# Kernel optimization log

Hardware: AMD Instinct MI355X
Metric: run time of the kernel (lower is better)

## Reference

```python
import jax, jax.numpy as jnp
import numpy as np

B, S, C, OUT = 8, 2048, 1024, 1024

def setup_inputs() -> dict:
    key = jax.random.key(0)
    ks = jax.random.split(key, 10)
    s = C ** -0.5
    return {
        "input": jax.random.normal(ks[0], (B, S, C), jnp.float32),
        "memory": jax.random.normal(ks[1], (B, S, C), jnp.float32),
        "Wq": jax.random.normal(ks[2], (C, C), jnp.float32) * s,
        "bq": jnp.zeros((C,), jnp.float32),
        "Wk": jax.random.normal(ks[3], (C, C), jnp.float32) * s,
        "bk": jnp.zeros((C,), jnp.float32),
        "Wv": jax.random.normal(ks[4], (C, C), jnp.float32) * s,
        "bv": jnp.zeros((C,), jnp.float32),
        "Wo": jax.random.normal(ks[5], (OUT, C), jnp.float32) * s,
        "bo": jnp.zeros((OUT,), jnp.float32),
    }

def reference(input, memory, Wq, bq, Wk, bk, Wv, bv, Wo, bo):
    depth_scale = input.shape[2] ** -0.5
    q = (input @ Wq.T + bq) * depth_scale          # [B, Sq, C]
    k = memory @ Wk.T + bk                          # [B, Sk, C]
    v = memory @ Wv.T + bv                          # [B, Sk, C]
    logit = jnp.einsum('bqc,bkc->bqk', q, k)        # [B, Sq, Sk]
    attn = jax.nn.softmax(logit, axis=-1)
    sel = jnp.einsum('bqk,bkc->bqc', attn, v)       # [B, Sq, C]
    return sel @ Wo.T + bo                          # [B, Sq, OUT]
```

## Files before the change

### kernel.cpp

```cpp
#include <hip/hip_runtime.h>
#include <hip/hip_bf16.h>


typedef __attribute__((ext_vector_type(8))) short short8;
typedef __attribute__((ext_vector_type(4))) float f32x4;

static __device__ __forceinline__ unsigned short f2bf(float f) {
  union { float f; unsigned u; } x; x.f = f;
  unsigned r = x.u + 0x7FFFu + ((x.u >> 16) & 1u);
  return (unsigned short)(r >> 16);
}

static __device__ __forceinline__ void g2l16(const void* g, void* l) {
  __builtin_amdgcn_global_load_lds(
      (const __attribute__((address_space(1))) void*)g,
      (__attribute__((address_space(3))) void*)l, 16, 0, 0);
}

__global__ __launch_bounds__(256) void cvt_kernel(const float* __restrict__ in,
                                                  unsigned short* __restrict__ out,
                                                  long long n4) {
  long long i = (long long)blockIdx.x * 256 + threadIdx.x;
  const long long stride = (long long)gridDim.x * 256;
  for (; i < n4; i += stride) {
    float4 v = ((const float4*)in)[i];
    ushort4 o;
    o.x = f2bf(v.x); o.y = f2bf(v.y); o.z = f2bf(v.z); o.w = f2bf(v.w);
    ((ushort4*)out)[i] = o;
  }
}

#define EPI_BF16 0
#define EPI_BF16_TRANS 1
#define EPI_EXP 2
#define EPI_PV 3
#define EPI_F32 4

template <int BM, int BN, int WM, int WN, int EPI, bool HAS_BIAS>
__global__ __launch_bounds__(512, 2) void gemm_kernel(
    const unsigned short* __restrict__ A, const unsigned short* __restrict__ B,
    const float* __restrict__ bias, void* __restrict__ Dv,
    int K, int lda, int ldb, int ldd,
    long long sA, long long sB, long long sD, float scale) {
  constexpr int MF = BM / (WM * 16);
  constexpr int NF = BN / (WN * 16);
  constexpr int LA = BM / 128;
  constexpr int LB = BN / 128;
  constexpr int LT = LA + LB;

  int lin = blockIdx.x + gridDim.x * (blockIdx.y + gridDim.y * blockIdx.z);
  const int nwg = gridDim.x * gridDim.y * gridDim.z;
  lin = (lin & 7) * (nwg >> 3) + (lin >> 3);
  const int bx = lin % gridDim.x;
  int rem0 = lin / gridDim.x;
  const int by = rem0 % gridDim.y;
  const int bz = rem0 / gridDim.y;

  const int bm = bx * BM;
  const int bn = by * BN;
  const int tid = threadIdx.x;
  const int lane = tid & 63;
  const int wid = tid >> 6;
  const int wr = (wid / WN) * (BM / WM);
  const int wc = (wid % WN) * (BN / WN);
  const int fr = lane & 15;
  const int hi = lane >> 4;

  __shared__ __align__(16) unsigned short As[4][BM * 32];
  __shared__ __align__(16) unsigned short Bs[4][BN * 32];

  f32x4 acc[MF][NF];
#pragma unroll
  for (int m = 0; m < MF; ++m)
#pragma unroll
    for (int n = 0; n < NF; ++n) acc[m][n] = (f32x4){0.f, 0.f, 0.f, 0.f};

  f32x4 asum[MF];
  short8 ones;
#pragma unroll
  for (int m = 0; m < MF; ++m) asum[m] = (f32x4){0.f, 0.f, 0.f, 0.f};
#pragma unroll
  for (int j = 0; j < 8; ++j) ones[j] = (short)0x3F80;

  const unsigned short* Abase = A + (long long)bz * sA;
  const unsigned short* Bbase = B + (long long)bz * sB;

  auto stage = [&](int tt) {
    const int buf = tt & 3;
#pragma unroll
    for (int i = 0; i < LA; ++i) {
      const int slot = i * 512 + tid;
      const int row = slot >> 2;
      const int gs = (slot & 3) ^ ((row >> 1) & 3);
      g2l16(Abase + (long long)(bm + row) * lda + tt * 32 + gs * 8,
            &As[buf][slot * 8]);
    }
#pragma unroll
    for (int i = 0; i < LB; ++i) {
      const int slot = i * 512 + tid;
      const int row = slot >> 2;
      const int gs = (slot & 3) ^ ((row >> 1) & 3);
      g2l16(Bbase + (long long)(bn + row) * ldb + tt * 32 + gs * 8,
            &Bs[buf][slot * 8]);
    }
  };

  const int NT = K >> 5;

  stage(0); stage(1); stage(2);

  const int glx = (fr >> 1) & 3;

  for (int t = 0; t < NT; ++t) {
    const int ahead = NT - 1 - t;
    if (ahead >= 2) {
      if (LT == 4) asm volatile("s_waitcnt vmcnt(8)" ::: "memory");
      else         asm volatile("s_waitcnt vmcnt(6)" ::: "memory");
    } else if (ahead == 1) {
      if (LT == 4) asm volatile("s_waitcnt vmcnt(4)" ::: "memory");
      else         asm volatile("s_waitcnt vmcnt(3)" ::: "memory");
    } else {
      asm volatile("s_waitcnt vmcnt(0)" ::: "memory");
    }
    __builtin_amdgcn_s_barrier();
    __builtin_amdgcn_sched_barrier(0);

    if (t + 3 < NT) stage(t + 3);

    const int buf = t & 3;
    short8 af[MF], bf[NF];
#pragma unroll
    for (int m = 0; m < MF; ++m) {
      const int row = wr + m * 16 + fr;
      af[m] = *(const short8*)&As[buf][row * 32 + ((hi ^ glx) << 3)];
    }
#pragma unroll
    for (int n = 0; n < NF; ++n) {
      const int row = wc + n * 16 + fr;
      bf[n] = *(const short8*)&Bs[buf][row * 32 + ((hi ^ glx) << 3)];
    }
#pragma unroll
    for (int m = 0; m < MF; ++m)
#pragma unroll
      for (int n = 0; n < NF; ++n)
        acc[m][n] = __builtin_amdgcn_mfma_f32_16x16x32_bf16(af[m], bf[n],
                                                            acc[m][n], 0, 0, 0);
    if (EPI == EPI_PV) {
#pragma unroll
      for (int m = 0; m < MF; ++m)
        asum[m] = __builtin_amdgcn_mfma_f32_16x16x32_bf16(af[m], ones,
                                                          asum[m], 0, 0, 0);
    }
    __builtin_amdgcn_sched_barrier(0);
    __builtin_amdgcn_s_barrier();
  }

  const int cr = hi * 4;
  const int cc = fr;
#pragma unroll
  for (int m = 0; m < MF; ++m) {
    const int row0 = bm + wr + m * 16 + cr;
#pragma unroll
    for (int n = 0; n < NF; ++n) {
      const int col = bn + wc + n * 16 + cc;
      const float bv = HAS_BIAS ? bias[col] : 0.f;
      if (EPI == EPI_F32) {
        float* D = (float*)Dv + (long long)bz * sD;
#pragma unroll
        for (int j = 0; j < 4; ++j)
          D[(long long)(row0 + j) * ldd + col] = acc[m][n][j] + bv;
      } else if (EPI == EPI_BF16) {
        unsigned short* D = (unsigned short*)Dv + (long long)bz * sD;
#pragma unroll
        for (int j = 0; j < 4; ++j)
          D[(long long)(row0 + j) * ldd + col] = f2bf((acc[m][n][j] + bv) * scale);
      } else if (EPI == EPI_BF16_TRANS) {
        unsigned short* D = (unsigned short*)Dv + (long long)bz * sD;
        ushort4 pk;
        pk.x = f2bf((acc[m][n][0] + bv) * scale);
        pk.y = f2bf((acc[m][n][1] + bv) * scale);
        pk.z = f2bf((acc[m][n][2] + bv) * scale);
        pk.w = f2bf((acc[m][n][3] + bv) * scale);
        *(ushort4*)&D[(long long)col * ldd + row0] = pk;
      } else if (EPI == EPI_EXP) {
        unsigned short* D = (unsigned short*)Dv + (long long)bz * sD;
#pragma unroll
        for (int j = 0; j < 4; ++j)
          D[(long long)(row0 + j) * ldd + col] = f2bf(__expf(acc[m][n][j]));
      } else {
        unsigned short* D = (unsigned short*)Dv + (long long)bz * sD;
#pragma unroll
        for (int j = 0; j < 4; ++j) {
          const float li = 1.f / asum[m][j];
          D[(long long)(row0 + j) * ldd + col] = f2bf(acc[m][n][j] * li);
        }
      }
    }
  }
}

extern "C" void kernel_launch(void* const* d_in, const int* in_sizes, int n_in,
                              void* d_out, int out_size, void* d_ws, size_t ws_size,
                              hipStream_t stream) {
  (void)in_sizes; (void)n_in; (void)out_size;
  const float* input  = (const float*)d_in[0];
  const float* memory = (const float*)d_in[1];
  const float* Wq = (const float*)d_in[2];
  const float* bq = (const float*)d_in[3];
  const float* Wk = (const float*)d_in[4];
  const float* bk = (const float*)d_in[5];
  const float* Wv = (const float*)d_in[6];
  const float* bv = (const float*)d_in[7];
  const float* Wo = (const float*)d_in[8];
  const float* bo = (const float*)d_in[9];
  float* out = (float*)d_out;

  const int S = 2048, C = 1024;
  const int CB = 4;
  const long long BS = 16384;
  const long long N_IN = BS * C;
  const long long N_W  = (long long)C * C;

  char* p = (char*)d_ws;
  auto alloc = [&](size_t bytes) {
    char* r = p;
    p += (bytes + 255) & ~(size_t)255;
    return r;
  };
  unsigned short* wqb  = (unsigned short*)alloc(N_W * 2);
  unsigned short* wkb  = (unsigned short*)alloc(N_W * 2);
  unsigned short* wvb  = (unsigned short*)alloc(N_W * 2);
  unsigned short* wob  = (unsigned short*)alloc(N_W * 2);
  unsigned short* Qb   = (unsigned short*)alloc(N_IN * 2);
  unsigned short* Kb   = (unsigned short*)alloc(N_IN * 2);
  unsigned short* Xb   = (unsigned short*)alloc(N_IN * 2);
  if ((size_t)(p - (char*)d_ws) > ws_size) return;

  unsigned short* Vt  = (unsigned short*)d_out;
  unsigned short* inb = (unsigned short*)d_out + N_IN;
  unsigned short* memb = Xb;
  unsigned short* Pt   = Xb;

  cvt_kernel<<<1024, 256, 0, stream>>>(Wq, wqb, N_W / 4);
  cvt_kernel<<<1024, 256, 0, stream>>>(Wk, wkb, N_W / 4);
  cvt_kernel<<<1024, 256, 0, stream>>>(Wv, wvb, N_W / 4);
  cvt_kernel<<<1024, 256, 0, stream>>>(Wo, wob, N_W / 4);
  cvt_kernel<<<2048, 256, 0, stream>>>(memory, memb, N_IN / 4);
  cvt_kernel<<<2048, 256, 0, stream>>>(input,  inb,  N_IN / 4);

  const float depth_scale = 0.03125f;

  gemm_kernel<256, 256, 2, 4, EPI_BF16, true><<<dim3(64, 4, 1), 512, 0, stream>>>(
      memb, wkb, bk, Kb, C, C, C, C, 0, 0, 0, 1.0f);
  gemm_kernel<256, 256, 2, 4, EPI_BF16_TRANS, true><<<dim3(64, 4, 1), 512, 0, stream>>>(
      memb, wvb, bv, Vt, C, C, C, (int)BS, 0, 0, 0, 1.0f);
  gemm_kernel<256, 256, 2, 4, EPI_BF16, true><<<dim3(64, 4, 1), 512, 0, stream>>>(
      inb, wqb, bq, Qb, C, C, C, C, 0, 0, 0, depth_scale);

  for (int c = 0; c < 8 / CB; ++c) {
    const long long qoff = (long long)c * CB * S * C;
    gemm_kernel<256, 256, 2, 4, EPI_EXP, false><<<dim3(8, 8, CB), 512, 0, stream>>>(
        Qb + qoff, Kb + qoff, nullptr, Pt,
        C, C, C, S, (long long)S * C, (long long)S * C, (long long)S * S, 1.0f);
    gemm_kernel<256, 128, 4, 2, EPI_PV, false><<<dim3(8, 8, CB), 512, 0, stream>>>(
        Pt, Vt + (long long)c * CB * S, nullptr, Qb + qoff,
        S, S, (int)BS, C, (long long)S * S, (long long)S, (long long)S * C, 1.0f);
  }

  gemm_kernel<256, 256, 2, 4, EPI_F32, true><<<dim3(64, 4, 1), 512, 0, stream>>>(
      Qb, wob, bo, out, C, C, C, C, 0, 0, 0, 1.0f);
}
```

Measured before the change: 460.0 us.

## Split GEMM main loop into two half-phases interleaving staging with MFMA

The GEMM k-loop now issues the A-tile and B-tile global-to-LDS loads in separate phases, each followed by half of the MFMA work, with priority raised around the MFMA blocks and the vmcnt wait moved to the end of the iteration. Global pointers are precomputed and advanced incrementally to cut address arithmetic. The PV GEMM switches from a 256x128 tile with a 4x2 wave layout to 128x256 with 2x4, and the four weight conversions are merged into one launch. The goal is better overlap of memory traffic with matrix math and fewer launches, in exchange for an extra barrier per iteration.

Result: slower. 495.6 us (+7.7%).

```diff
diff --git a/kernel.cpp b/kernel.cpp
--- a/kernel.cpp
+++ b/kernel.cpp
@@ -15,6 +15,14 @@
   __builtin_amdgcn_global_load_lds(
       (const __attribute__((address_space(1))) void*)g,
       (__attribute__((address_space(3))) void*)l, 16, 0, 0);
+}
+
+template <int N> static __device__ __forceinline__ void vmw() {
+  if constexpr (N == 8)      asm volatile("s_waitcnt vmcnt(8)" ::: "memory");
+  else if constexpr (N == 6) asm volatile("s_waitcnt vmcnt(6)" ::: "memory");
+  else if constexpr (N == 4) asm volatile("s_waitcnt vmcnt(4)" ::: "memory");
+  else if constexpr (N == 3) asm volatile("s_waitcnt vmcnt(3)" ::: "memory");
+  else                       asm volatile("s_waitcnt vmcnt(0)" ::: "memory");
 }
 
 __global__ __launch_bounds__(256) void cvt_kernel(const float* __restrict__ in,
@@ -30,23 +38,50 @@
   }
 }
 
+__global__ __launch_bounds__(256) void wcvt_kernel(
+    const float* __restrict__ w0, const float* __restrict__ w1,
+    const float* __restrict__ w2, const float* __restrict__ w3,
+    unsigned short* __restrict__ o0, unsigned short* __restrict__ o1,
+    unsigned short* __restrict__ o2, unsigned short* __restrict__ o3,
+    int n4) {
+  const float* src; unsigned short* dst;
+  switch (blockIdx.y) {
+    case 0: src = w0; dst = o0; break;
+    case 1: src = w1; dst = o1; break;
+    case 2: src = w2; dst = o2; break;
+    default: src = w3; dst = o3; break;
+  }
+  int i = blockIdx.x * 256 + threadIdx.x;
+  const int stride = gridDim.x * 256;
+  for (; i < n4; i += stride) {
+    float4 v = ((const float4*)src)[i];
+    ushort4 o;
+    o.x = f2bf(v.x); o.y = f2bf(v.y); o.z = f2bf(v.z); o.w = f2bf(v.w);
+    ((ushort4*)dst)[i] = o;
+  }
+}
+
 #define EPI_BF16 0
 #define EPI_BF16_TRANS 1
 #define EPI_EXP 2
 #define EPI_PV 3
 #define EPI_F32 4
 
-template <int BM, int BN, int WM, int WN, int EPI, bool HAS_BIAS>
+template <int BM, int BN, int EPI, bool HAS_BIAS>
 __global__ __launch_bounds__(512, 2) void gemm_kernel(
     const unsigned short* __restrict__ A, const unsigned short* __restrict__ B,
     const float* __restrict__ bias, void* __restrict__ Dv,
     int K, int lda, int ldb, int ldd,
     long long sA, long long sB, long long sD, float scale) {
+  constexpr int WM = 2, WN = 4;
   constexpr int MF = BM / (WM * 16);
   constexpr int NF = BN / (WN * 16);
+  constexpr int MH = MF / 2;
   constexpr int LA = BM / 128;
   constexpr int LB = BN / 128;
   constexpr int LT = LA + LB;
+  constexpr int ASL = BM * 32;
+  constexpr int BSL = BN * 32;
 
   int lin = blockIdx.x + gridDim.x * (blockIdx.y + gridDim.y * blockIdx.z);
   const int nwg = gridDim.x * gridDim.y * gridDim.z;
@@ -65,9 +100,10 @@
   const int wc = (wid % WN) * (BN / WN);
   const int fr = lane & 15;
   const int hi = lane >> 4;
-
-  __shared__ __align__(16) unsigned short As[4][BM * 32];
-  __shared__ __align__(16) unsigned short Bs[4][BN * 32];
+  const int rg = ((hi ^ ((fr >> 1) & 3)) << 3);
+
+  __shared__ __align__(16) unsigned short As[4 * ASL];
+  __shared__ __align__(16) unsigned short Bs[4 * BSL];
 
   f32x4 acc[MF][NF];
 #pragma unroll
@@ -82,77 +118,108 @@
 #pragma unroll
   for (int j = 0; j < 8; ++j) ones[j] = (short)0x3F80;
 
-  const unsigned short* Abase = A + (long long)bz * sA;
-  const unsigned short* Bbase = B + (long long)bz * sB;
-
-  auto stage = [&](int tt) {
-    const int buf = tt & 3;
+  const unsigned short* apt[LA];
+  const unsigned short* bpt[LB];
+#pragma unroll
+  for (int i = 0; i < LA; ++i) {
+    const int slot = i * 512 + tid;
+    const int row = slot >> 2;
+    const int g = (slot & 3) ^ ((row >> 1) & 3);
+    apt[i] = A + (long long)bz * sA + (long long)(bm + row) * lda + g * 8;
+  }
+#pragma unroll
+  for (int i = 0; i < LB; ++i) {
+    const int slot = i * 512 + tid;
+    const int row = slot >> 2;
+    const int g = (slot & 3) ^ ((row >> 1) & 3);
+    bpt[i] = B + (long long)bz * sB + (long long)(bn + row) * ldb + g * 8;
+  }
+  auto stageA = [&](int buf) {
 #pragma unroll
     for (int i = 0; i < LA; ++i) {
-      const int slot = i * 512 + tid;
-      const int row = slot >> 2;
-      const int gs = (slot & 3) ^ ((row >> 1) & 3);
-      g2l16(Abase + (long long)(bm + row) * lda + tt * 32 + gs * 8,
-            &As[buf][slot * 8]);
-    }
+      g2l16(apt[i], &As[buf * ASL + (i * 512 + tid) * 8]);
+      apt[i] += 32;
+    }
+  };
+  auto stageB = [&](int buf) {
 #pragma unroll
     for (int i = 0; i < LB; ++i) {
-      const int slot = i * 512 + tid;
-      const int row = slot >> 2;
-      const int gs = (slot & 3) ^ ((row >> 1) & 3);
-      g2l16(Bbase + (long long)(bn + row) * ldb + tt * 32 + gs * 8,
-            &Bs[buf][slot * 8]);
+      g2l16(bpt[i], &Bs[buf * BSL + (i * 512 + tid) * 8]);
+      bpt[i] += 32;
     }
   };
 
   const int NT = K >> 5;
 
-  stage(0); stage(1); stage(2);
-
-  const int glx = (fr >> 1) & 3;
+  stageA(0); stageB(0);
+  stageA(1); stageB(1);
+  stageA(2); stageB(2);
+  vmw<2 * LT>();
+  __builtin_amdgcn_s_barrier();
+  __builtin_amdgcn_sched_barrier(0);
 
   for (int t = 0; t < NT; ++t) {
-    const int ahead = NT - 1 - t;
-    if (ahead >= 2) {
-      if (LT == 4) asm volatile("s_waitcnt vmcnt(8)" ::: "memory");
-      else         asm volatile("s_waitcnt vmcnt(6)" ::: "memory");
-    } else if (ahead == 1) {
-      if (LT == 4) asm volatile("s_waitcnt vmcnt(4)" ::: "memory");
-      else         asm volatile("s_waitcnt vmcnt(3)" ::: "memory");
-    } else {
-      asm volatile("s_waitcnt vmcnt(0)" ::: "memory");
-    }
+    const int buf = t & 3;
+    const int nbuf = (t + 3) & 3;
+    const bool st = (t + 3) < NT;
+
+    if (st) stageA(nbuf);
+    short8 af0[MH], bf[NF];
+#pragma unroll
+    for (int m = 0; m < MH; ++m)
+      af0[m] = *(const short8*)&As[buf * ASL + (wr + m * 16 + fr) * 32 + rg];
+#pragma unroll
+    for (int n = 0; n < NF; ++n)
+      bf[n] = *(const short8*)&Bs[buf * BSL + (wc + n * 16 + fr) * 32 + rg];
+    __builtin_amdgcn_sched_barrier(0);
     __builtin_amdgcn_s_barrier();
     __builtin_amdgcn_sched_barrier(0);
-
-    if (t + 3 < NT) stage(t + 3);
-
-    const int buf = t & 3;
-    short8 af[MF], bf[NF];
-#pragma unroll
-    for (int m = 0; m < MF; ++m) {
-      const int row = wr + m * 16 + fr;
-      af[m] = *(const short8*)&As[buf][row * 32 + ((hi ^ glx) << 3)];
-    }
-#pragma unroll
-    for (int n = 0; n < NF; ++n) {
-      const int row = wc + n * 16 + fr;
-      bf[n] = *(const short8*)&Bs[buf][row * 32 + ((hi ^ glx) << 3)];
-    }
-#pragma unroll
-    for (int m = 0; m < MF; ++m)
+    __builtin_amdgcn_s_setprio(1);
+#pragma unroll
+    for (int m = 0; m < MH; ++m)
 #pragma unroll
       for (int n = 0; n < NF; ++n)
-        acc[m][n] = __builtin_amdgcn_mfma_f32_16x16x32_bf16(af[m], bf[n],
+        acc[m][n] = __builtin_amdgcn_mfma_f32_16x16x32_bf16(af0[m], bf[n],
                                                             acc[m][n], 0, 0, 0);
     if (EPI == EPI_PV) {
 #pragma unroll
-      for (int m = 0; m < MF; ++m)
-        asum[m] = __builtin_amdgcn_mfma_f32_16x16x32_bf16(af[m], ones,
+      for (int m = 0; m < MH; ++m)
+        asum[m] = __builtin_amdgcn_mfma_f32_16x16x32_bf16(af0[m], ones,
                                                           asum[m], 0, 0, 0);
     }
+    __builtin_amdgcn_s_setprio(0);
     __builtin_amdgcn_sched_barrier(0);
     __builtin_amdgcn_s_barrier();
+    __builtin_amdgcn_sched_barrier(0);
+
+    if (st) stageB(nbuf);
+    short8 af1[MH];
+#pragma unroll
+    for (int m = 0; m < MH; ++m)
+      af1[m] = *(const short8*)&As[buf * ASL + (wr + (MH + m) * 16 + fr) * 32 + rg];
+    __builtin_amdgcn_sched_barrier(0);
+    __builtin_amdgcn_s_barrier();
+    __builtin_amdgcn_sched_barrier(0);
+    __builtin_amdgcn_s_setprio(1);
+#pragma unroll
+    for (int m = 0; m < MH; ++m)
+#pragma unroll
+      for (int n = 0; n < NF; ++n)
+        acc[MH + m][n] = __builtin_amdgcn_mfma_f32_16x16x32_bf16(af1[m], bf[n],
+                                                                 acc[MH + m][n], 0, 0, 0);
+    if (EPI == EPI_PV) {
+#pragma unroll
+      for (int m = 0; m < MH; ++m)
+        asum[MH + m] = __builtin_amdgcn_mfma_f32_16x16x32_bf16(af1[m], ones,
+                                                               asum[MH + m], 0, 0, 0);
+    }
+    __builtin_amdgcn_s_setprio(0);
+    __builtin_amdgcn_sched_barrier(0);
+    if (t + 3 < NT)       vmw<2 * LT>();
+    else if (t + 2 < NT)  vmw<LT>();
+    else if (t + 1 < NT)  vmw<0>();
+    __builtin_amdgcn_s_barrier();
+    __builtin_amdgcn_sched_barrier(0);
   }
 
   const int cr = hi * 4;
@@ -241,32 +308,31 @@
   unsigned short* memb = Xb;
   unsigned short* Pt   = Xb;
 
-  cvt_kernel<<<1024, 256, 0, stream>>>(Wq, wqb, N_W / 4);
-  cvt_kernel<<<1024, 256, 0, stream>>>(Wk, wkb, N_W / 4);
-  cvt_kernel<<<1024, 256, 0, stream>>>(Wv, wvb, N_W / 4);
-  cvt_kernel<<<1024, 256, 0, stream>>>(Wo, wob, N_W / 4);
+  wcvt_kernel<<<dim3(256, 4, 1), 256, 0, stream>>>(Wq, Wk, Wv, Wo,
+                                                   wqb, wkb, wvb, wob,
+                                                   (int)(N_W / 4));
   cvt_kernel<<<2048, 256, 0, stream>>>(memory, memb, N_IN / 4);
   cvt_kernel<<<2048, 256, 0, stream>>>(input,  inb,  N_IN / 4);
 
   const float depth_scale = 0.03125f;
 
-  gemm_kernel<256, 256, 2, 4, EPI_BF16, true><<<dim3(64, 4, 1), 512, 0, stream>>>(
+  gemm_kernel<256, 256, EPI_BF16, true><<<dim3(64, 4, 1), 512, 0, stream>>>(
       memb, wkb, bk, Kb, C, C, C, C, 0, 0, 0, 1.0f);
-  gemm_kernel<256, 256, 2, 4, EPI_BF16_TRANS, true><<<dim3(64, 4, 1), 512, 0, stream>>>(
+  gemm_kernel<256, 256, EPI_BF16_TRANS, true><<<dim3(64, 4, 1), 512, 0, stream>>>(
       memb, wvb, bv, Vt, C, C, C, (int)BS, 0, 0, 0, 1.0f);
-  gemm_kernel<256, 256, 2, 4, EPI_BF16, true><<<dim3(64, 4, 1), 512, 0, stream>>>(
+  gemm_kernel<256, 256, EPI_BF16, true><<<dim3(64, 4, 1), 512, 0, stream>>>(
       inb, wqb, bq, Qb, C, C, C, C, 0, 0, 0, depth_scale);
 
   for (int c = 0; c < 8 / CB; ++c) {
     const long long qoff = (long long)c * CB * S * C;
-    gemm_kernel<256, 256, 2, 4, EPI_EXP, false><<<dim3(8, 8, CB), 512, 0, stream>>>(
+    gemm_kernel<256, 256, EPI_EXP, false><<<dim3(8, 8, CB), 512, 0, stream>>>(
         Qb + qoff, Kb + qoff, nullptr, Pt,
         C, C, C, S, (long long)S * C, (long long)S * C, (long long)S * S, 1.0f);
-    gemm_kernel<256, 128, 4, 2, EPI_PV, false><<<dim3(8, 8, CB), 512, 0, stream>>>(
+    gemm_kernel<128, 256, EPI_PV, false><<<dim3(16, 4, CB), 512, 0, stream>>>(
         Pt, Vt + (long long)c * CB * S, nullptr, Qb + qoff,
         S, S, (int)BS, C, (long long)S * S, (long long)S, (long long)S * C, 1.0f);
   }
 
-  gemm_kernel<256, 256, 2, 4, EPI_F32, true><<<dim3(64, 4, 1), 512, 0, stream>>>(
+  gemm_kernel<256, 256, EPI_F32, true><<<dim3(64, 4, 1), 512, 0, stream>>>(
       Qb, wob, bo, out, C, C, C, C, 0, 0, 0, 1.0f);
 }
```
